# Kernel tuning notes

Hardware: AMD Instinct MI355X
Metric: run time of the kernel (lower is better)

## Reference

```python
import jax, jax.numpy as jnp
import numpy as np

QLEN, MLEN, BSZ, D_MODEL, N_HEAD, D_HEAD = 1024, 1024, 4, 1024, 16, 64
KLEN = QLEN + MLEN
LN_EPS = 1e-5


def _linear(x, W, b):
    return x @ W + b


def _layer_norm(x, g, b):
    mu = jnp.mean(x, axis=-1, keepdims=True)
    var = jnp.var(x, axis=-1, keepdims=True)
    return (x - mu) * jax.lax.rsqrt(var + LN_EPS) * g + b


def _rel_shift(x):
    # x: [b, n, q, k] -> Transformer-XL rel-shift via zero-pad + reshape trick
    b, n, q, k = x.shape
    x = jnp.pad(x, ((0, 0), (0, 0), (0, 0), (1, 0)))
    x = x.reshape(b, n, k + 1, q)[:, :, 1:, :].reshape(b, n, q, k)
    return x


def setup_inputs() -> dict:
    key = jax.random.key(0)
    ks = jax.random.split(key, 16)
    s = 0.02
    inp = {
        "w": jax.random.normal(ks[0], (QLEN, BSZ, D_MODEL), jnp.float32),
        "r": jax.random.normal(ks[1], (KLEN, D_MODEL), jnp.float32),
        "r_w_bias": jax.random.normal(ks[2], (N_HEAD, D_HEAD), jnp.float32) * s,
        "r_r_bias": jax.random.normal(ks[3], (N_HEAD, D_HEAD), jnp.float32) * s,
        "mems": jax.random.normal(ks[4], (MLEN, BSZ, D_MODEL), jnp.float32),
        "Wq": jax.random.normal(ks[5], (D_MODEL, N_HEAD * D_HEAD), jnp.float32) * s,
        "bq": jnp.zeros((N_HEAD * D_HEAD,), jnp.float32),
        "Wk": jax.random.normal(ks[6], (D_MODEL, N_HEAD * D_HEAD), jnp.float32) * s,
        "bk": jnp.zeros((N_HEAD * D_HEAD,), jnp.float32),
        "Wv": jax.random.normal(ks[7], (D_MODEL, N_HEAD * D_HEAD), jnp.float32) * s,
        "bv": jnp.zeros((N_HEAD * D_HEAD,), jnp.float32),
        "Wr": jax.random.normal(ks[8], (D_MODEL, N_HEAD * D_HEAD), jnp.float32) * s,
        "br": jnp.zeros((N_HEAD * D_HEAD,), jnp.float32),
        "Wo": jax.random.normal(ks[9], (N_HEAD * D_HEAD, D_MODEL), jnp.float32) * s,
        "bo": jnp.zeros((D_MODEL,), jnp.float32),
        "ln_g": jnp.ones((D_MODEL,), jnp.float32),
        "ln_b": jnp.zeros((D_MODEL,), jnp.float32),
    }
    # causal mask with memory: key j visible to query i iff j <= i + MLEN
    inp["attn_mask"] = jnp.arange(KLEN)[None, :] > (jnp.arange(QLEN)[:, None] + MLEN)
    return inp


def reference(w, r, r_w_bias, r_r_bias, mems, Wq, bq, Wk, bk, Wv, bv, Wr, br,
              Wo, bo, ln_g, ln_b, attn_mask):
    qlen, bsz = w.shape[0], w.shape[1]
    scale = 1.0 / (D_HEAD ** 0.5)

    cat = jnp.concatenate([mems, w], axis=0)               # [klen, b, d]
    klen = cat.shape[0]

    q = _linear(cat, Wq, bq)[-qlen:]                       # [q, b, n*d]
    k = _linear(cat, Wk, bk)                               # [k, b, n*d]
    v = _linear(cat, Wv, bv)
    rk = _linear(r, Wr, br)                                # [rlen, n*d]

    q = q.reshape(qlen, bsz, N_HEAD, D_HEAD)
    k = k.reshape(klen, bsz, N_HEAD, D_HEAD)
    v = v.reshape(klen, bsz, N_HEAD, D_HEAD)
    rk = rk.reshape(r.shape[0], N_HEAD, D_HEAD)

    AC = jnp.einsum('ibnd,jbnd->bnij', q + r_w_bias, k)
    BD = jnp.einsum('ibnd,jnd->bnij', q + r_r_bias, rk)
    BD = _rel_shift(BD)

    attn_score = scale * (AC + BD)                          # [b, n, q, k]
    attn_score = jnp.where(attn_mask[None, None, :, :], -jnp.inf, attn_score)
    attn_prob = jax.nn.softmax(attn_score, axis=3)

    attn_vec = jnp.einsum('bnij,jbnd->ibnd', attn_prob, v)
    attn_vec = attn_vec.reshape(qlen, bsz, N_HEAD * D_HEAD)
    attn_out = _linear(attn_vec, Wo, bo)

    return _layer_norm(w + attn_out, ln_g, ln_b)            # post-lnorm path
```

## Files before the change

kernel.cpp:

```cpp
#include <hip/hip_runtime.h>
#include <stdint.h>


typedef unsigned short u16;
typedef unsigned int u32;
typedef __attribute__((ext_vector_type(8))) short s16x8;
typedef __attribute__((ext_vector_type(4))) float f32x4;

typedef const __attribute__((address_space(1))) void gvoid;
typedef __attribute__((address_space(3))) void lvoid;

__device__ __forceinline__ void async16(const u16* g, u16* l) {
  __builtin_amdgcn_global_load_lds((gvoid*)g, (lvoid*)l, 16, 0, 0);
}

__device__ __forceinline__ float b2f(u16 h) {
  union { u32 u; float f; } v; v.u = ((u32)h) << 16; return v.f;
}
__device__ __forceinline__ u16 f2b(float f) {
  union { float f; u32 u; } v; v.f = f; u32 u = v.u;
  return (u16)((u + 0x7FFFu + ((u >> 16) & 1u)) >> 16);
}
__device__ __forceinline__ bool is_bf16(const u16* lng) { return lng[0] == 0x3F80u; }

__device__ __forceinline__ void ld8(const void* p, size_t idx, bool bf, u16* dst) {
  if (bf) {
    *(uint4*)dst = *(const uint4*)((const u16*)p + idx);
  } else {
    const float* f = (const float*)p + idx;
    float4 a = *(const float4*)f;
    float4 c = *(const float4*)(f + 4);
    dst[0] = f2b(a.x); dst[1] = f2b(a.y); dst[2] = f2b(a.z); dst[3] = f2b(a.w);
    dst[4] = f2b(c.x); dst[5] = f2b(c.y); dst[6] = f2b(c.z); dst[7] = f2b(c.w);
  }
}
__device__ __forceinline__ float ldS(const void* p, int idx, bool bf) {
  return bf ? b2f(((const u16*)p)[idx]) : ((const float*)p)[idx];
}

__device__ __forceinline__ void gemm_bt_body(
    u16* As, u16* Bs,
    const void* Alo, const void* Ahi, int splitRow,
    const u16* BT, const void* bias,
    const void* eb0, const void* eb1,
    u16* C0, u16* C1, bool bfin, bool abf,
    int bm, int bnc)
{
  const int t = threadIdx.x;
  const int lane = t & 63, w = t >> 6;
  const int wr = w >> 1, wc = w & 1;
  const int ml = lane & 15, q = lane >> 4;

  f32x4 zero4 = {0.f, 0.f, 0.f, 0.f};
  f32x4 acc[4][4];
#pragma unroll
  for (int i = 0; i < 4; ++i)
#pragma unroll
    for (int j = 0; j < 4; ++j) acc[i][j] = zero4;

  const int srow = t >> 3;
  const int scol = (((t & 7) ^ ((t >> 3) & 7)) << 3);
  const void* aptr[4]; size_t aidx[4]; const u16* bsrc[4];
#pragma unroll
  for (int p = 0; p < 4; ++p) {
    int gr = bm + p * 32 + srow;
    if (gr < splitRow) { aptr[p] = Alo; aidx[p] = (size_t)gr * 1024 + scol; }
    else { aptr[p] = Ahi; aidx[p] = (size_t)(gr - splitRow) * 1024 + scol; }
    bsrc[p] = BT + (size_t)(bnc + p * 32 + srow) * 1024 + scol;
  }

  for (int kk = 0; kk < 1024; kk += 64) {
    if (abf) {
      __syncthreads();
#pragma unroll
      for (int p = 0; p < 4; ++p) {
        async16((const u16*)aptr[p] + aidx[p] + kk, As + p * 2048 + t * 8);
        async16(bsrc[p] + kk, Bs + p * 2048 + t * 8);
      }
      __syncthreads();
    } else {
      u16 ta[4][8]; uint4 tb[4];
#pragma unroll
      for (int p = 0; p < 4; ++p) {
        ld8(aptr[p], aidx[p] + kk, false, ta[p]);
        tb[p] = *(const uint4*)(bsrc[p] + kk);
      }
      __syncthreads();
#pragma unroll
      for (int p = 0; p < 4; ++p) {
        *(uint4*)(As + p * 2048 + t * 8) = *(uint4*)ta[p];
        *(uint4*)(Bs + p * 2048 + t * 8) = tb[p];
      }
      __syncthreads();
    }
#pragma unroll
    for (int ki = 0; ki < 2; ++ki) {
      s16x8 af[4], bf[4];
#pragma unroll
      for (int mi = 0; mi < 4; ++mi) {
        int row = wr * 64 + mi * 16 + ml;
        af[mi] = *(const s16x8*)&As[row * 64 + ((((ki << 2) + q) ^ (ml & 7)) << 3)];
      }
#pragma unroll
      for (int ni = 0; ni < 4; ++ni) {
        int row = wc * 64 + ni * 16 + ml;
        bf[ni] = *(const s16x8*)&Bs[row * 64 + ((((ki << 2) + q) ^ (ml & 7)) << 3)];
      }
#pragma unroll
      for (int mi = 0; mi < 4; ++mi)
#pragma unroll
        for (int ni = 0; ni < 4; ++ni)
          acc[mi][ni] = __builtin_amdgcn_mfma_f32_16x16x32_bf16(af[mi], bf[ni],
                                                                acc[mi][ni], 0, 0, 0);
    }
  }

#pragma unroll
  for (int ni = 0; ni < 4; ++ni) {
    int gcol = bnc + wc * 64 + ni * 16 + ml;
    float bi = ldS(bias, gcol, bfin);
    float e0 = eb0 ? ldS(eb0, gcol, bfin) : 0.f;
    float e1 = eb1 ? ldS(eb1, gcol, bfin) : 0.f;
#pragma unroll
    for (int mi = 0; mi < 4; ++mi)
#pragma unroll
      for (int rr = 0; rr < 4; ++rr) {
        int grow = bm + wr * 64 + mi * 16 + 4 * q + rr;
        size_t off = (size_t)grow * 1024 + gcol;
        float v0 = acc[mi][ni][rr] + bi;
        if (C1) { C0[off] = f2b(v0 + e0); C1[off] = f2b(v0 + e1); }
        else    { C0[off] = f2b(v0); }
      }
  }
}

__device__ __forceinline__ void gemm_vt_body(
    u16* As, u16* Bs,
    const void* Mlo, const void* Whi,
    const u16* WvT, const void* bv,
    u16* vT, bool bfin,
    int j0, int nc0, int b)
{
  const int t = threadIdx.x;
  const int lane = t & 63, w = t >> 6;
  const int wr = w >> 1, wc = w & 1;
  const int ml = lane & 15, q = lane >> 4;

  f32x4 zero4 = {0.f, 0.f, 0.f, 0.f};
  f32x4 acc[4][4];
#pragma unroll
  for (int i = 0; i < 4; ++i)
#pragma unroll
    for (int j = 0; j < 4; ++j) acc[i][j] = zero4;

  const int srow = t >> 3;
  const int scol = (((t & 7) ^ ((t >> 3) & 7)) << 3);
  const u16* asrc[4]; const void* bptr[4]; size_t bidx[4];
#pragma unroll
  for (int p = 0; p < 4; ++p) {
    asrc[p] = WvT + (size_t)(nc0 + p * 32 + srow) * 1024 + scol;
    int j = j0 + p * 32 + srow;
    if (j < 1024) { bptr[p] = Mlo; bidx[p] = ((size_t)j * 4 + b) * 1024 + scol; }
    else { bptr[p] = Whi; bidx[p] = ((size_t)(j - 1024) * 4 + b) * 1024 + scol; }
  }

  for (int kk = 0; kk < 1024; kk += 64) {
    if (bfin) {
      __syncthreads();
#pragma unroll
      for (int p = 0; p < 4; ++p) {
        async16(asrc[p] + kk, As + p * 2048 + t * 8);
        async16((const u16*)bptr[p] + bidx[p] + kk, Bs + p * 2048 + t * 8);
      }
      __syncthreads();
    } else {
      u16 tb[4][8];
#pragma unroll
      for (int p = 0; p < 4; ++p) ld8(bptr[p], bidx[p] + kk, false, tb[p]);
      __syncthreads();
#pragma unroll
      for (int p = 0; p < 4; ++p) {
        async16(asrc[p] + kk, As + p * 2048 + t * 8);
        *(uint4*)(Bs + p * 2048 + t * 8) = *(uint4*)tb[p];
      }
      __syncthreads();
    }
#pragma unroll
    for (int ki = 0; ki < 2; ++ki) {
      s16x8 af[4], bf[4];
#pragma unroll
      for (int mi = 0; mi < 4; ++mi) {
        int row = wr * 64 + mi * 16 + ml;
        af[mi] = *(const s16x8*)&As[row * 64 + ((((ki << 2) + q) ^ (ml & 7)) << 3)];
      }
#pragma unroll
      for (int ni = 0; ni < 4; ++ni) {
        int row = wc * 64 + ni * 16 + ml;
        bf[ni] = *(const s16x8*)&Bs[row * 64 + ((((ki << 2) + q) ^ (ml & 7)) << 3)];
      }
#pragma unroll
      for (int mi = 0; mi < 4; ++mi)
#pragma unroll
        for (int ni = 0; ni < 4; ++ni)
          acc[mi][ni] = __builtin_amdgcn_mfma_f32_16x16x32_bf16(af[mi], bf[ni],
                                                                acc[mi][ni], 0, 0, 0);
    }
  }

#pragma unroll
  for (int mi = 0; mi < 4; ++mi)
#pragma unroll
    for (int rr = 0; rr < 4; ++rr) {
      int nc = nc0 + wr * 64 + mi * 16 + 4 * q + rr;
      float bi = ldS(bv, nc, bfin);
      size_t rbase = ((size_t)b * 1024 + nc) * 2048 + j0 + wc * 64 + ml * 4;
      u32 w0 = (u32)f2b(acc[mi][0][rr] + bi) | ((u32)f2b(acc[mi][1][rr] + bi) << 16);
      u32 w1 = (u32)f2b(acc[mi][2][rr] + bi) | ((u32)f2b(acc[mi][3][rr] + bi) << 16);
      uint2 pk; pk.x = w0; pk.y = w1;
      *(uint2*)(vT + rbase) = pk;
    }
}

__global__ __launch_bounds__(256) void gemm_bt(
    const void* __restrict__ Alo, const void* __restrict__ Ahi, int splitRow,
    const u16* __restrict__ BT, const void* __restrict__ bias,
    const void* __restrict__ eb0, const void* __restrict__ eb1,
    u16* __restrict__ C0, u16* __restrict__ C1,
    const u16* __restrict__ lng, int aIsInput)
{
  __shared__ u16 As[128 * 64];
  __shared__ u16 Bs[128 * 64];
  const bool bfin = is_bf16(lng);
  const bool abf = aIsInput ? bfin : true;
  gemm_bt_body(As, Bs, Alo, Ahi, splitRow, BT, bias, eb0, eb1, C0, C1,
               bfin, abf, blockIdx.y * 128, blockIdx.x * 128);
}

__global__ __launch_bounds__(256) void proj_uber(
    const void* __restrict__ mems, const void* __restrict__ w,
    const void* __restrict__ r,
    const u16* __restrict__ WkT, const void* __restrict__ bk,
    const u16* __restrict__ WvT, const void* __restrict__ bv,
    const u16* __restrict__ WqT, const void* __restrict__ bq,
    const void* __restrict__ rwb, const void* __restrict__ rrb,
    const u16* __restrict__ WrT, const void* __restrict__ br,
    u16* __restrict__ kb, u16* __restrict__ vT,
    u16* __restrict__ qw, u16* __restrict__ qr, u16* __restrict__ rkb,
    const u16* __restrict__ lng)
{
  __shared__ u16 As[128 * 64];
  __shared__ u16 Bs[128 * 64];
  const bool bfin = is_bf16(lng);
  int id = blockIdx.x;
  id = (id & 7) * 176 + (id >> 3);

  if (id < 512) {
    int bx = id & 7, by = id >> 3;
    gemm_bt_body(As, Bs, mems, w, 4096, WkT, bk, nullptr, nullptr,
                 kb, nullptr, bfin, bfin, by * 128, bx * 128);
  } else if (id < 1024) {
    int local = id - 512;
    int jx = local & 15, ny = (local >> 4) & 7, b = local >> 7;
    gemm_vt_body(As, Bs, mems, w, WvT, bv, vT, bfin, jx * 128, ny * 128, b);
  } else if (id < 1280) {
    int local = id - 1024;
    int bx = local & 7, by = local >> 3;
    gemm_bt_body(As, Bs, w, w, 4096, WqT, bq, rwb, rrb,
                 qw, qr, bfin, bfin, by * 128, bx * 128);
  } else {
    int local = id - 1280;
    int bx = local & 7, by = local >> 3;
    gemm_bt_body(As, Bs, r, r, 1 << 30, WrT, br, nullptr, nullptr,
                 rkb, nullptr, bfin, bfin, by * 128, bx * 128);
  }
}

__global__ __launch_bounds__(256) void transpose_w5(
    const void* __restrict__ W0, const void* __restrict__ W1,
    const void* __restrict__ W2, const void* __restrict__ W3,
    const void* __restrict__ W4,
    u16* __restrict__ T0, u16* __restrict__ T1, u16* __restrict__ T2,
    u16* __restrict__ T3, u16* __restrict__ T4, const u16* __restrict__ lng)
{
  __shared__ u16 tile[64 * 72];
  const bool bf = is_bf16(lng);
  const void* W; u16* T;
  switch (blockIdx.z) {
    case 0: W = W0; T = T0; break;
    case 1: W = W1; T = T1; break;
    case 2: W = W2; T = T2; break;
    case 3: W = W3; T = T3; break;
    default: W = W4; T = T4; break;
  }
  const int t = threadIdx.x;
  const int k0 = blockIdx.y * 64, n0 = blockIdx.x * 64;
#pragma unroll
  for (int p = 0; p < 2; ++p) {
    int s = p * 256 + t, row = s >> 3, ch = s & 7;
    u16 tmp[8];
    ld8(W, (size_t)(k0 + row) * 1024 + n0 + ch * 8, bf, tmp);
    *(uint4*)&tile[row * 72 + ch * 8] = *(uint4*)tmp;
  }
  __syncthreads();
#pragma unroll
  for (int p = 0; p < 2; ++p) {
    int s = p * 256 + t, nrow = s >> 3, ch = s & 7;
    union { u16 u[8]; uint4 v; } pk;
#pragma unroll
    for (int jj = 0; jj < 8; ++jj) pk.u[jj] = tile[(ch * 8 + jj) * 72 + nrow];
    *(uint4*)(T + (size_t)(n0 + nrow) * 1024 + k0 + ch * 8) = pk.v;
  }
}

__global__ __launch_bounds__(512, 4) void flash_attn(
    const u16* __restrict__ qw, const u16* __restrict__ qr,
    const u16* __restrict__ kb, const u16* __restrict__ vt,
    const u16* __restrict__ rkb, u16* __restrict__ av)
{
  constexpr int LP = 72;
  __shared__ u16 Ks[64 * LP];
  __shared__ u16 Vs[64 * LP];
  __shared__ u16 Rs[192 * LP];
  __shared__ u16 Ps[8][16 * LP];

  const int t = threadIdx.x;
  const int lane = t & 63, w = t >> 6;
  const int ml = lane & 15, q = lane >> 4;
  const int hbid = blockIdx.y * 8 + blockIdx.x;
  const int lbid = (hbid & 7) * 64 + (hbid >> 3);
  const int L = lbid & 63;
  const int i0idx = (L < 32) ? (L & 7) : 7 - (L & 7);
  const int i0 = i0idx * 128;
  const int bn = lbid >> 3, b = bn >> 4, nh = bn & 15;

  s16x8 aqw[2], aqr[2];
  {
    size_t qo = ((size_t)(i0 + 16 * w + ml) * 4 + b) * 1024 + nh * 64 + q * 8;
    aqw[0] = *(const s16x8*)(qw + qo);
    aqw[1] = *(const s16x8*)(qw + qo + 32);
    aqr[0] = *(const s16x8*)(qr + qo);
    aqr[1] = *(const s16x8*)(qr + qo + 32);
  }

  f32x4 zero4 = {0.f, 0.f, 0.f, 0.f};
  f32x4 o[4];
#pragma unroll
  for (int dt = 0; dt < 4; ++dt) o[dt] = zero4;
  float lsum[4] = {0.f, 0.f, 0.f, 0.f};

  const int ntiles = min(i0 / 64 + 18, 32);
  const int c_lo = 16 * (7 - w);
  const int srow = t >> 3, sch = t & 7;

  uint4 pK, pV, pR;
  auto issue_kv = [&](int jt) {
    const int j0n = jt * 64;
    pK = *(const uint4*)(kb + ((size_t)(j0n + srow) * 4 + b) * 1024 + nh * 64 + sch * 8);
    pV = *(const uint4*)(vt + ((size_t)bn * 64 + srow) * 2048 + j0n + sch * 8);
  };
  auto rload = [&](int g) {
    g = g < 0 ? 0 : (g > 2047 ? 2047 : g);
    return *(const uint4*)(rkb + (size_t)g * 1024 + nh * 64 + sch * 8);
  };

  {
    issue_kv(0);
    uint4 r0 = rload(896 - i0 + srow);
    uint4 r1 = rload(896 - i0 + srow + 64);
    uint4 r2 = rload(896 - i0 + srow + 128);
    *(uint4*)&Ks[srow * LP + sch * 8] = pK;
    *(uint4*)&Vs[srow * LP + sch * 8] = pV;
    *(uint4*)&Rs[(srow      ) * LP + sch * 8] = r0;
    *(uint4*)&Rs[(srow +  64) * LP + sch * 8] = r1;
    *(uint4*)&Rs[(srow + 128) * LP + sch * 8] = r2;
  }
  __syncthreads();

  int slab = 0;
  int rbase = c_lo;
  for (int jt = 0; jt < ntiles; ++jt) {
    const int j0 = jt * 64;
    if (jt > 0) {
      __syncthreads();
      *(uint4*)&Ks[srow * LP + sch * 8] = pK;
      *(uint4*)&Vs[srow * LP + sch * 8] = pV;
      *(uint4*)&Rs[(slab * 64 + srow) * LP + sch * 8] = pR;
      slab = slab == 2 ? 0 : slab + 1;
      rbase += 64; if (rbase >= 192) rbase -= 192;
      __syncthreads();
    }
    if (jt + 1 < ntiles) {
      issue_kv(jt + 1);
      pR = rload(64 * jt + 1088 - i0 + srow);
    }

    f32x4 sac[4];
#pragma unroll
    for (int tt = 0; tt < 4; ++tt) sac[tt] = zero4;
#pragma unroll
    for (int ki = 0; ki < 2; ++ki)
#pragma unroll
      for (int tt = 0; tt < 4; ++tt) {
        s16x8 bfr = *(const s16x8*)&Ks[(tt * 16 + ml) * LP + ki * 32 + q * 8];
        sac[tt] = __builtin_amdgcn_mfma_f32_16x16x32_bf16(aqw[ki], bfr, sac[tt], 0, 0, 0);
      }

    f32x4 g[5];
#pragma unroll
    for (int ct = 0; ct < 5; ++ct) g[ct] = zero4;
#pragma unroll
    for (int ct = 0; ct < 5; ++ct) {
      int pb = rbase + ct * 16; if (pb >= 192) pb -= 192;
      const u16* rp = &Rs[(pb + ml) * LP + q * 8];
      s16x8 b0 = *(const s16x8*)(rp);
      s16x8 b1 = *(const s16x8*)(rp + 32);
      g[ct] = __builtin_amdgcn_mfma_f32_16x16x32_bf16(aqr[0], b0, g[ct], 0, 0, 0);
      g[ct] = __builtin_amdgcn_mfma_f32_16x16x32_bf16(aqr[1], b1, g[ct], 0, 0, 0);
    }

    const bool mtile = (j0 + 63) > (i0 + 1024);

#pragma unroll
    for (int rr = 0; rr < 4; ++rr) {
      const int r = 4 * q + rr;
      const int irow = i0 + 16 * w + r;
      const int L2 = ((ml - r + 15) & 15) | (q << 4);
      const bool hs = ml < 15 - r;
      float bl0 = hs ? g[1][rr] : g[0][rr];
      float bl1 = hs ? g[2][rr] : g[1][rr];
      float bl2 = hs ? g[3][rr] : g[2][rr];
      float bl3 = hs ? g[4][rr] : g[3][rr];
      float band0 = __shfl(bl0, L2, 64);
      float band1 = __shfl(bl1, L2, 64);
      float band2 = __shfl(bl2, L2, 64);
      float band3 = __shfl(bl3, L2, 64);
      float s0 = 0.125f * (sac[0][rr] + band0);
      float s1 = 0.125f * (sac[1][rr] + band1);
      float s2 = 0.125f * (sac[2][rr] + band2);
      float s3 = 0.125f * (sac[3][rr] + band3);
      if (mtile) {
        int lim = irow + 1024 - j0 - ml;
        if (0 > lim)  s0 = -3.0e38f;
        if (16 > lim) s1 = -3.0e38f;
        if (32 > lim) s2 = -3.0e38f;
        if (48 > lim) s3 = -3.0e38f;
      }
      float p0 = __expf(s0), p1 = __expf(s1), p2 = __expf(s2), p3 = __expf(s3);
      lsum[rr] += (p0 + p1) + (p2 + p3);
      u32 w0 = (u32)f2b(p0) | ((u32)f2b(p1) << 16);
      u32 w1 = (u32)f2b(p2) | ((u32)f2b(p3) << 16);
      uint2 pk; pk.x = w0; pk.y = w1;
      *(uint2*)&Ps[w][r * LP + ml * 4] = pk;
    }

#pragma unroll
    for (int ki = 0; ki < 2; ++ki) {
      s16x8 a = *(const s16x8*)&Ps[w][ml * LP + ki * 32 + q * 8];
#pragma unroll
      for (int dt = 0; dt < 4; ++dt) {
        s16x8 bfr = *(const s16x8*)&Vs[(dt * 16 + ml) * LP + ki * 32 + q * 8];
        o[dt] = __builtin_amdgcn_mfma_f32_16x16x32_bf16(a, bfr, o[dt], 0, 0, 0);
      }
    }
  }

#pragma unroll
  for (int rr = 0; rr < 4; ++rr) {
    float l = lsum[rr];
#pragma unroll
    for (int off = 1; off < 16; off <<= 1) l += __shfl_xor(l, off);
    float inv = 1.f / l;
    int i = i0 + 16 * w + 4 * q + rr;
#pragma unroll
    for (int dt = 0; dt < 4; ++dt)
      av[((size_t)i * 4 + b) * 1024 + nh * 64 + dt * 16 + ml] = f2b(o[dt][rr] * inv);
  }
}

__global__ __launch_bounds__(256) void ln_kernel(
    const void* __restrict__ wi, const u16* __restrict__ ao,
    const void* __restrict__ gg, const void* __restrict__ bb,
    void* __restrict__ out)
{
  __shared__ float red[8];
  const bool bf = is_bf16((const u16*)gg);
  const int t = threadIdx.x;
  const int row = blockIdx.x;
  const int base = row * 1024 + t * 4;
  float x0, x1, x2, x3;
  if (bf) {
    ushort4 xw = *(const ushort4*)((const u16*)wi + base);
    x0 = b2f(xw.x); x1 = b2f(xw.y); x2 = b2f(xw.z); x3 = b2f(xw.w);
  } else {
    float4 xw = *(const float4*)((const float*)wi + base);
    x0 = xw.x; x1 = xw.y; x2 = xw.z; x3 = xw.w;
  }
  ushort4 xa = *(const ushort4*)(ao + base);
  x0 += b2f(xa.x); x1 += b2f(xa.y); x2 += b2f(xa.z); x3 += b2f(xa.w);
  float s = x0 + x1 + x2 + x3;
  float s2 = x0 * x0 + x1 * x1 + x2 * x2 + x3 * x3;
#pragma unroll
  for (int off = 1; off < 64; off <<= 1) {
    s += __shfl_xor(s, off);
    s2 += __shfl_xor(s2, off);
  }
  if ((t & 63) == 0) { red[t >> 6] = s; red[4 + (t >> 6)] = s2; }
  __syncthreads();
  float S = red[0] + red[1] + red[2] + red[3];
  float S2 = red[4] + red[5] + red[6] + red[7];
  float mu = S * (1.f / 1024.f);
  float var = S2 * (1.f / 1024.f) - mu * mu;
  float inv = rsqrtf(var + 1e-5f);
  float g0 = ldS(gg, t * 4 + 0, bf), g1 = ldS(gg, t * 4 + 1, bf);
  float g2 = ldS(gg, t * 4 + 2, bf), g3 = ldS(gg, t * 4 + 3, bf);
  float b0 = ldS(bb, t * 4 + 0, bf), b1 = ldS(bb, t * 4 + 1, bf);
  float b2v = ldS(bb, t * 4 + 2, bf), b3 = ldS(bb, t * 4 + 3, bf);
  float y0 = (x0 - mu) * inv * g0 + b0;
  float y1 = (x1 - mu) * inv * g1 + b1;
  float y2 = (x2 - mu) * inv * g2 + b2v;
  float y3 = (x3 - mu) * inv * g3 + b3;
  if (bf) {
    ushort4 r;
    r.x = f2b(y0); r.y = f2b(y1); r.z = f2b(y2); r.w = f2b(y3);
    *(ushort4*)((u16*)out + base) = r;
  } else {
    float4 r; r.x = y0; r.y = y1; r.z = y2; r.w = y3;
    *(float4*)((float*)out + base) = r;
  }
}

__global__ __launch_bounds__(256) void copy_w(
    const void* __restrict__ wi, const u16* __restrict__ lng,
    void* __restrict__ out)
{
  const bool bf = is_bf16(lng);
  int i = blockIdx.x * 256 + threadIdx.x;
  if (bf) ((u16*)out)[i] = ((const u16*)wi)[i];
  else    ((float*)out)[i] = ((const float*)wi)[i];
}

extern "C" void kernel_launch(void* const* d_in, const int* in_sizes, int n_in,
                              void* d_out, int out_size, void* d_ws, size_t ws_size,
                              hipStream_t stream) {
  (void)in_sizes; (void)n_in; (void)out_size;
  const void* w    = d_in[0];
  const void* r    = d_in[1];
  const void* rwb  = d_in[2];
  const void* rrb  = d_in[3];
  const void* mems = d_in[4];
  const void* Wq   = d_in[5];
  const void* bq   = d_in[6];
  const void* Wk   = d_in[7];
  const void* bk   = d_in[8];
  const void* Wv   = d_in[9];
  const void* bv   = d_in[10];
  const void* Wr   = d_in[11];
  const void* br   = d_in[12];
  const void* Wo   = d_in[13];
  const void* bo   = d_in[14];
  const u16*  lng  = (const u16*)d_in[15];
  const void* lnb  = d_in[16];

  dim3 blk(256);
  const size_t M = (size_t)1 << 20;
  const size_t NEED = 31 * M * 2;
  if (ws_size < NEED) {
    copy_w<<<dim3(16384), blk, 0, stream>>>(w, lng, d_out);
    return;
  }

  u16* ws  = (u16*)d_ws;
  u16* WqT = ws + 0 * M;
  u16* WkT = ws + 1 * M;
  u16* WvT = ws + 2 * M;
  u16* WrT = ws + 3 * M;
  u16* WoT = ws + 4 * M;
  u16* kb  = ws + 5 * M;
  u16* vT  = ws + 13 * M;
  u16* qw  = ws + 21 * M;
  u16* qr  = ws + 25 * M;
  u16* rkb = ws + 29 * M;
  u16* av  = ws + 0 * M;
  u16* ao  = qw;

  transpose_w5<<<dim3(16, 16, 5), blk, 0, stream>>>(Wq, Wk, Wv, Wr, Wo,
                                                    WqT, WkT, WvT, WrT, WoT, lng);
  proj_uber<<<dim3(1408), blk, 0, stream>>>(mems, w, r,
                                            WkT, bk, WvT, bv, WqT, bq, rwb, rrb,
                                            WrT, br, kb, vT, qw, qr, rkb, lng);
  flash_attn<<<dim3(8, 64), dim3(512), 0, stream>>>(qw, qr, kb, vT, rkb, av);
  gemm_bt<<<dim3(8, 32), blk, 0, stream>>>(av, av, 1 << 30, WoT, bo,
                                           nullptr, nullptr, ao, nullptr, lng, 0);
  ln_kernel<<<dim3(4096), blk, 0, stream>>>(w, ao, lng, lnb, d_out);
}
```

Baseline: 403.9 us.

## Use 256x256 tiles for projection GEMMs, retile output GEMM, add MFMA priority hints

```diff
diff --git a/kernel.cpp b/kernel.cpp
--- a/kernel.cpp
+++ b/kernel.cpp
@@ -38,7 +38,7 @@
   return bf ? b2f(((const u16*)p)[idx]) : ((const float*)p)[idx];
 }
 
-__device__ __forceinline__ void gemm_bt_body(
+__device__ __forceinline__ void gemm256_bt_body(
     u16* As, u16* Bs,
     const void* Alo, const void* Ahi, int splitRow,
     const u16* BT, const void* bias,
@@ -48,36 +48,38 @@
 {
   const int t = threadIdx.x;
   const int lane = t & 63, w = t >> 6;
-  const int wr = w >> 1, wc = w & 1;
+  const int wm = w >> 2, wn = w & 3;
   const int ml = lane & 15, q = lane >> 4;
 
   f32x4 zero4 = {0.f, 0.f, 0.f, 0.f};
-  f32x4 acc[4][4];
-#pragma unroll
-  for (int i = 0; i < 4; ++i)
+  f32x4 acc[8][4];
+#pragma unroll
+  for (int i = 0; i < 8; ++i)
 #pragma unroll
     for (int j = 0; j < 4; ++j) acc[i][j] = zero4;
 
   const int srow = t >> 3;
-  const int scol = (((t & 7) ^ ((t >> 3) & 7)) << 3);
+  const int scol = ((t & 7) ^ ((t >> 3) & 7)) << 3;
   const void* aptr[4]; size_t aidx[4]; const u16* bsrc[4];
 #pragma unroll
   for (int p = 0; p < 4; ++p) {
-    int gr = bm + p * 32 + srow;
+    int gr = bm + p * 64 + srow;
     if (gr < splitRow) { aptr[p] = Alo; aidx[p] = (size_t)gr * 1024 + scol; }
     else { aptr[p] = Ahi; aidx[p] = (size_t)(gr - splitRow) * 1024 + scol; }
-    bsrc[p] = BT + (size_t)(bnc + p * 32 + srow) * 1024 + scol;
-  }
+    bsrc[p] = BT + (size_t)(bnc + p * 64 + srow) * 1024 + scol;
+  }
+  u16* lA[4]; u16* lB[4];
+#pragma unroll
+  for (int p = 0; p < 4; ++p) { lA[p] = As + p * 4096 + t * 8; lB[p] = Bs + p * 4096 + t * 8; }
 
   for (int kk = 0; kk < 1024; kk += 64) {
+    __syncthreads();
     if (abf) {
-      __syncthreads();
 #pragma unroll
       for (int p = 0; p < 4; ++p) {
-        async16((const u16*)aptr[p] + aidx[p] + kk, As + p * 2048 + t * 8);
-        async16(bsrc[p] + kk, Bs + p * 2048 + t * 8);
-      }
-      __syncthreads();
+        async16((const u16*)aptr[p] + aidx[p] + kk, lA[p]);
+        async16(bsrc[p] + kk, lB[p]);
+      }
     } else {
       u16 ta[4][8]; uint4 tb[4];
 #pragma unroll
@@ -85,29 +87,25 @@
         ld8(aptr[p], aidx[p] + kk, false, ta[p]);
         tb[p] = *(const uint4*)(bsrc[p] + kk);
       }
-      __syncthreads();
 #pragma unroll
       for (int p = 0; p < 4; ++p) {
-        *(uint4*)(As + p * 2048 + t * 8) = *(uint4*)ta[p];
-        *(uint4*)(Bs + p * 2048 + t * 8) = tb[p];
-      }
-      __syncthreads();
-    }
+        *(uint4*)lA[p] = *(uint4*)ta[p];
+        *(uint4*)lB[p] = tb[p];
+      }
+    }
+    __syncthreads();
 #pragma unroll
     for (int ki = 0; ki < 2; ++ki) {
-      s16x8 af[4], bf[4];
-#pragma unroll
-      for (int mi = 0; mi < 4; ++mi) {
-        int row = wr * 64 + mi * 16 + ml;
-        af[mi] = *(const s16x8*)&As[row * 64 + ((((ki << 2) + q) ^ (ml & 7)) << 3)];
-      }
-#pragma unroll
-      for (int ni = 0; ni < 4; ++ni) {
-        int row = wc * 64 + ni * 16 + ml;
-        bf[ni] = *(const s16x8*)&Bs[row * 64 + ((((ki << 2) + q) ^ (ml & 7)) << 3)];
-      }
-#pragma unroll
-      for (int mi = 0; mi < 4; ++mi)
+      const int rc = (((ki << 2) + q) ^ (ml & 7)) << 3;
+      s16x8 af[8], bf[4];
+#pragma unroll
+      for (int mi = 0; mi < 8; ++mi)
+        af[mi] = *(const s16x8*)&As[(wm * 128 + mi * 16 + ml) * 64 + rc];
+#pragma unroll
+      for (int ni = 0; ni < 4; ++ni)
+        bf[ni] = *(const s16x8*)&Bs[(wn * 64 + ni * 16 + ml) * 64 + rc];
+#pragma unroll
+      for (int mi = 0; mi < 8; ++mi)
 #pragma unroll
         for (int ni = 0; ni < 4; ++ni)
           acc[mi][ni] = __builtin_amdgcn_mfma_f32_16x16x32_bf16(af[mi], bf[ni],
@@ -117,15 +115,15 @@
 
 #pragma unroll
   for (int ni = 0; ni < 4; ++ni) {
-    int gcol = bnc + wc * 64 + ni * 16 + ml;
+    int gcol = bnc + wn * 64 + ni * 16 + ml;
     float bi = ldS(bias, gcol, bfin);
     float e0 = eb0 ? ldS(eb0, gcol, bfin) : 0.f;
     float e1 = eb1 ? ldS(eb1, gcol, bfin) : 0.f;
 #pragma unroll
-    for (int mi = 0; mi < 4; ++mi)
+    for (int mi = 0; mi < 8; ++mi)
 #pragma unroll
       for (int rr = 0; rr < 4; ++rr) {
-        int grow = bm + wr * 64 + mi * 16 + 4 * q + rr;
+        int grow = bm + wm * 128 + mi * 16 + 4 * q + rr;
         size_t off = (size_t)grow * 1024 + gcol;
         float v0 = acc[mi][ni][rr] + bi;
         if (C1) { C0[off] = f2b(v0 + e0); C1[off] = f2b(v0 + e1); }
@@ -134,7 +132,7 @@
   }
 }
 
-__device__ __forceinline__ void gemm_vt_body(
+__device__ __forceinline__ void gemm256_vt_body(
     u16* As, u16* Bs,
     const void* Mlo, const void* Whi,
     const u16* WvT, const void* bv,
@@ -143,63 +141,61 @@
 {
   const int t = threadIdx.x;
   const int lane = t & 63, w = t >> 6;
-  const int wr = w >> 1, wc = w & 1;
+  const int wm = w >> 2, wn = w & 3;
   const int ml = lane & 15, q = lane >> 4;
 
   f32x4 zero4 = {0.f, 0.f, 0.f, 0.f};
-  f32x4 acc[4][4];
-#pragma unroll
-  for (int i = 0; i < 4; ++i)
+  f32x4 acc[8][4];
+#pragma unroll
+  for (int i = 0; i < 8; ++i)
 #pragma unroll
     for (int j = 0; j < 4; ++j) acc[i][j] = zero4;
 
   const int srow = t >> 3;
-  const int scol = (((t & 7) ^ ((t >> 3) & 7)) << 3);
+  const int scol = ((t & 7) ^ ((t >> 3) & 7)) << 3;
   const u16* asrc[4]; const void* bptr[4]; size_t bidx[4];
 #pragma unroll
   for (int p = 0; p < 4; ++p) {
-    asrc[p] = WvT + (size_t)(nc0 + p * 32 + srow) * 1024 + scol;
-    int j = j0 + p * 32 + srow;
+    asrc[p] = WvT + (size_t)(nc0 + p * 64 + srow) * 1024 + scol;
+    int j = j0 + p * 64 + srow;
     if (j < 1024) { bptr[p] = Mlo; bidx[p] = ((size_t)j * 4 + b) * 1024 + scol; }
     else { bptr[p] = Whi; bidx[p] = ((size_t)(j - 1024) * 4 + b) * 1024 + scol; }
   }
+  u16* lA[4]; u16* lB[4];
+#pragma unroll
+  for (int p = 0; p < 4; ++p) { lA[p] = As + p * 4096 + t * 8; lB[p] = Bs + p * 4096 + t * 8; }
 
   for (int kk = 0; kk < 1024; kk += 64) {
+    __syncthreads();
     if (bfin) {
-      __syncthreads();
 #pragma unroll
       for (int p = 0; p < 4; ++p) {
-        async16(asrc[p] + kk, As + p * 2048 + t * 8);
-        async16((const u16*)bptr[p] + bidx[p] + kk, Bs + p * 2048 + t * 8);
-      }
-      __syncthreads();
+        async16(asrc[p] + kk, lA[p]);
+        async16((const u16*)bptr[p] + bidx[p] + kk, lB[p]);
+      }
     } else {
       u16 tb[4][8];
 #pragma unroll
       for (int p = 0; p < 4; ++p) ld8(bptr[p], bidx[p] + kk, false, tb[p]);
-      __syncthreads();
 #pragma unroll
       for (int p = 0; p < 4; ++p) {
-        async16(asrc[p] + kk, As + p * 2048 + t * 8);
-        *(uint4*)(Bs + p * 2048 + t * 8) = *(uint4*)tb[p];
-      }
-      __syncthreads();
-    }
+        async16(asrc[p] + kk, lA[p]);
+        *(uint4*)lB[p] = *(uint4*)tb[p];
+      }
+    }
+    __syncthreads();
 #pragma unroll
     for (int ki = 0; ki < 2; ++ki) {
-      s16x8 af[4], bf[4];
-#pragma unroll
-      for (int mi = 0; mi < 4; ++mi) {
-        int row = wr * 64 + mi * 16 + ml;
-        af[mi] = *(const s16x8*)&As[row * 64 + ((((ki << 2) + q) ^ (ml & 7)) << 3)];
-      }
-#pragma unroll
-      for (int ni = 0; ni < 4; ++ni) {
-        int row = wc * 64 + ni * 16 + ml;
-        bf[ni] = *(const s16x8*)&Bs[row * 64 + ((((ki << 2) + q) ^ (ml & 7)) << 3)];
-      }
-#pragma unroll
-      for (int mi = 0; mi < 4; ++mi)
+      const int rc = (((ki << 2) + q) ^ (ml & 7)) << 3;
+      s16x8 af[8], bf[4];
+#pragma unroll
+      for (int mi = 0; mi < 8; ++mi)
+        af[mi] = *(const s16x8*)&As[(wm * 128 + mi * 16 + ml) * 64 + rc];
+#pragma unroll
+      for (int ni = 0; ni < 4; ++ni)
+        bf[ni] = *(const s16x8*)&Bs[(wn * 64 + ni * 16 + ml) * 64 + rc];
+#pragma unroll
+      for (int mi = 0; mi < 8; ++mi)
 #pragma unroll
         for (int ni = 0; ni < 4; ++ni)
           acc[mi][ni] = __builtin_amdgcn_mfma_f32_16x16x32_bf16(af[mi], bf[ni],
@@ -208,12 +204,12 @@
   }
 
 #pragma unroll
-  for (int mi = 0; mi < 4; ++mi)
+  for (int mi = 0; mi < 8; ++mi)
 #pragma unroll
     for (int rr = 0; rr < 4; ++rr) {
-      int nc = nc0 + wr * 64 + mi * 16 + 4 * q + rr;
+      int nc = nc0 + wm * 128 + mi * 16 + 4 * q + rr;
       float bi = ldS(bv, nc, bfin);
-      size_t rbase = ((size_t)b * 1024 + nc) * 2048 + j0 + wc * 64 + ml * 4;
+      size_t rbase = ((size_t)b * 1024 + nc) * 2048 + j0 + wn * 64 + ml * 4;
       u32 w0 = (u32)f2b(acc[mi][0][rr] + bi) | ((u32)f2b(acc[mi][1][rr] + bi) << 16);
       u32 w1 = (u32)f2b(acc[mi][2][rr] + bi) | ((u32)f2b(acc[mi][3][rr] + bi) << 16);
       uint2 pk; pk.x = w0; pk.y = w1;
@@ -221,22 +217,7 @@
     }
 }
 
-__global__ __launch_bounds__(256) void gemm_bt(
-    const void* __restrict__ Alo, const void* __restrict__ Ahi, int splitRow,
-    const u16* __restrict__ BT, const void* __restrict__ bias,
-    const void* __restrict__ eb0, const void* __restrict__ eb1,
-    u16* __restrict__ C0, u16* __restrict__ C1,
-    const u16* __restrict__ lng, int aIsInput)
-{
-  __shared__ u16 As[128 * 64];
-  __shared__ u16 Bs[128 * 64];
-  const bool bfin = is_bf16(lng);
-  const bool abf = aIsInput ? bfin : true;
-  gemm_bt_body(As, Bs, Alo, Ahi, splitRow, BT, bias, eb0, eb1, C0, C1,
-               bfin, abf, blockIdx.y * 128, blockIdx.x * 128);
-}
-
-__global__ __launch_bounds__(256) void proj_uber(
+__global__ __launch_bounds__(512, 2) void proj_uber256(
     const void* __restrict__ mems, const void* __restrict__ w,
     const void* __restrict__ r,
     const u16* __restrict__ WkT, const void* __restrict__ bk,
@@ -248,31 +229,139 @@
     u16* __restrict__ qw, u16* __restrict__ qr, u16* __restrict__ rkb,
     const u16* __restrict__ lng)
 {
-  __shared__ u16 As[128 * 64];
-  __shared__ u16 Bs[128 * 64];
+  __shared__ u16 As[256 * 64];
+  __shared__ u16 Bs[256 * 64];
   const bool bfin = is_bf16(lng);
   int id = blockIdx.x;
-  id = (id & 7) * 176 + (id >> 3);
-
-  if (id < 512) {
-    int bx = id & 7, by = id >> 3;
-    gemm_bt_body(As, Bs, mems, w, 4096, WkT, bk, nullptr, nullptr,
-                 kb, nullptr, bfin, bfin, by * 128, bx * 128);
-  } else if (id < 1024) {
-    int local = id - 512;
-    int jx = local & 15, ny = (local >> 4) & 7, b = local >> 7;
-    gemm_vt_body(As, Bs, mems, w, WvT, bv, vT, bfin, jx * 128, ny * 128, b);
-  } else if (id < 1280) {
-    int local = id - 1024;
-    int bx = local & 7, by = local >> 3;
-    gemm_bt_body(As, Bs, w, w, 4096, WqT, bq, rwb, rrb,
-                 qw, qr, bfin, bfin, by * 128, bx * 128);
+  id = (id & 7) * 44 + (id >> 3);
+
+  if (id < 128) {
+    int bx = id & 3, by = id >> 2;
+    gemm256_bt_body(As, Bs, mems, w, 4096, WkT, bk, nullptr, nullptr,
+                    kb, nullptr, bfin, bfin, by * 256, bx * 256);
+  } else if (id < 256) {
+    int local = id - 128;
+    int jx = local & 7, ny = (local >> 3) & 3, b = local >> 5;
+    gemm256_vt_body(As, Bs, mems, w, WvT, bv, vT, bfin, jx * 256, ny * 256, b);
+  } else if (id < 320) {
+    int local = id - 256;
+    int bx = local & 3, by = local >> 2;
+    gemm256_bt_body(As, Bs, w, w, 1 << 30, WqT, bq, rwb, rrb,
+                    qw, qr, bfin, bfin, by * 256, bx * 256);
   } else {
-    int local = id - 1280;
-    int bx = local & 7, by = local >> 3;
-    gemm_bt_body(As, Bs, r, r, 1 << 30, WrT, br, nullptr, nullptr,
-                 rkb, nullptr, bfin, bfin, by * 128, bx * 128);
-  }
+    int local = id - 320;
+    int bx = local & 3, by = local >> 2;
+    gemm256_bt_body(As, Bs, r, r, 1 << 30, WrT, br, nullptr, nullptr,
+                    rkb, nullptr, bfin, bfin, by * 256, bx * 256);
+  }
+}
+
+__device__ __forceinline__ void gemm_bt_body(
+    u16* As, u16* Bs,
+    const void* Alo, const void* Ahi, int splitRow,
+    const u16* BT, const void* bias,
+    const void* eb0, const void* eb1,
+    u16* C0, u16* C1, bool bfin, bool abf,
+    int bm, int bnc)
+{
+  const int t = threadIdx.x;
+  const int lane = t & 63, w = t >> 6;
+  const int wr = w >> 1, wc = w & 1;
+  const int ml = lane & 15, q = lane >> 4;
+
+  f32x4 zero4 = {0.f, 0.f, 0.f, 0.f};
+  f32x4 acc[4][4];
+#pragma unroll
+  for (int i = 0; i < 4; ++i)
+#pragma unroll
+    for (int j = 0; j < 4; ++j) acc[i][j] = zero4;
+
+  const int srow = t >> 2;
+  const int sch  = t & 3;
+  const void* aptr[2]; size_t aidx[2]; const u16* bsrc[2];
+#pragma unroll
+  for (int p = 0; p < 2; ++p) {
+    int gr = bm + srow + p * 64;
+    if (gr < splitRow) { aptr[p] = Alo; aidx[p] = (size_t)gr * 1024 + sch * 8; }
+    else { aptr[p] = Ahi; aidx[p] = (size_t)(gr - splitRow) * 1024 + sch * 8; }
+    bsrc[p] = BT + (size_t)(bnc + srow + p * 64) * 1024 + sch * 8;
+  }
+  u16* lA[2] = { As + t * 8, As + 2048 + t * 8 };
+  u16* lB[2] = { Bs + t * 8, Bs + 2048 + t * 8 };
+
+  for (int kk = 0; kk < 1024; kk += 32) {
+    if (abf) {
+      __syncthreads();
+      async16((const u16*)aptr[0] + aidx[0] + kk, lA[0]);
+      async16((const u16*)aptr[1] + aidx[1] + kk, lA[1]);
+      async16(bsrc[0] + kk, lB[0]);
+      async16(bsrc[1] + kk, lB[1]);
+      __syncthreads();
+    } else {
+      u16 ta0[8], ta1[8];
+      ld8(aptr[0], aidx[0] + kk, false, ta0);
+      ld8(aptr[1], aidx[1] + kk, false, ta1);
+      uint4 vb0 = *(const uint4*)(bsrc[0] + kk);
+      uint4 vb1 = *(const uint4*)(bsrc[1] + kk);
+      __syncthreads();
+      *(uint4*)lA[0] = *(uint4*)ta0;
+      *(uint4*)lA[1] = *(uint4*)ta1;
+      *(uint4*)lB[0] = vb0;
+      *(uint4*)lB[1] = vb1;
+      __syncthreads();
+    }
+    s16x8 af[4], bf[4];
+#pragma unroll
+    for (int mi = 0; mi < 4; ++mi)
+      af[mi] = *(const s16x8*)&As[(wr * 64 + mi * 16 + ml) * 32 + q * 8];
+#pragma unroll
+    for (int ni = 0; ni < 4; ++ni)
+      bf[ni] = *(const s16x8*)&Bs[(wc * 64 + ni * 16 + ml) * 32 + q * 8];
+#pragma unroll
+    for (int mi = 0; mi < 4; ++mi)
+#pragma unroll
+      for (int ni = 0; ni < 4; ++ni)
+        acc[mi][ni] = __builtin_amdgcn_mfma_f32_16x16x32_bf16(af[mi], bf[ni],
+                                                              acc[mi][ni], 0, 0, 0);
+  }
+
+#pragma unroll
+  for (int ni = 0; ni < 4; ++ni) {
+    int gcol = bnc + wc * 64 + ni * 16 + ml;
+    float bi = ldS(bias, gcol, bfin);
+    float e0 = eb0 ? ldS(eb0, gcol, bfin) : 0.f;
+    float e1 = eb1 ? ldS(eb1, gcol, bfin) : 0.f;
+#pragma unroll
+    for (int mi = 0; mi < 4; ++mi)
+#pragma unroll
+      for (int rr = 0; rr < 4; ++rr) {
+        int grow = bm + wr * 64 + mi * 16 + 4 * q + rr;
+        size_t off = (size_t)grow * 1024 + gcol;
+        float v0 = acc[mi][ni][rr] + bi;
+        if (C1) { C0[off] = f2b(v0 + e0); C1[off] = f2b(v0 + e1); }
+        else    { C0[off] = f2b(v0); }
+      }
+  }
+}
+
+__global__ __launch_bounds__(256) void gemm_bt(
+    const void* __restrict__ Alo, const void* __restrict__ Ahi, int splitRow,
+    const u16* __restrict__ BT, const void* __restrict__ bias,
+    const void* __restrict__ eb0, const void* __restrict__ eb1,
+    u16* __restrict__ C0, u16* __restrict__ C1,
+    const u16* __restrict__ lng, int aIsInput)
+{
+  __shared__ u16 As[128 * 32];
+  __shared__ u16 Bs[128 * 32];
+  const bool bfin = is_bf16(lng);
+  const bool abf = aIsInput ? bfin : true;
+  int lin = blockIdx.y * gridDim.x + blockIdx.x;
+  int nwg = gridDim.x * gridDim.y;
+  int cpx = nwg >> 3;
+  int id  = (lin & 7) * cpx + (lin >> 3);
+  int bx = id % gridDim.x, by = id / gridDim.x;
+  gemm_bt_body(As, Bs, Alo, Ahi, splitRow, BT, bias, eb0, eb1, C0, C1,
+               bfin, abf, by * 128, bx * 128);
 }
 
 __global__ __launch_bounds__(256) void transpose_w5(
@@ -394,6 +483,7 @@
       pR = rload(64 * jt + 1088 - i0 + srow);
     }
 
+    __builtin_amdgcn_s_setprio(1);
     f32x4 sac[4];
 #pragma unroll
     for (int tt = 0; tt < 4; ++tt) sac[tt] = zero4;
@@ -417,6 +507,7 @@
       g[ct] = __builtin_amdgcn_mfma_f32_16x16x32_bf16(aqr[0], b0, g[ct], 0, 0, 0);
       g[ct] = __builtin_amdgcn_mfma_f32_16x16x32_bf16(aqr[1], b1, g[ct], 0, 0, 0);
     }
+    __builtin_amdgcn_s_setprio(0);
 
     const bool mtile = (j0 + 63) > (i0 + 1024);
 
@@ -453,6 +544,7 @@
       *(uint2*)&Ps[w][r * LP + ml * 4] = pk;
     }
 
+    __builtin_amdgcn_s_setprio(1);
 #pragma unroll
     for (int ki = 0; ki < 2; ++ki) {
       s16x8 a = *(const s16x8*)&Ps[w][ml * LP + ki * 32 + q * 8];
@@ -462,6 +554,7 @@
         o[dt] = __builtin_amdgcn_mfma_f32_16x16x32_bf16(a, bfr, o[dt], 0, 0, 0);
       }
     }
+    __builtin_amdgcn_s_setprio(0);
   }
 
 #pragma unroll
@@ -585,9 +678,10 @@
 
   transpose_w5<<<dim3(16, 16, 5), blk, 0, stream>>>(Wq, Wk, Wv, Wr, Wo,
                                                     WqT, WkT, WvT, WrT, WoT, lng);
-  proj_uber<<<dim3(1408), blk, 0, stream>>>(mems, w, r,
-                                            WkT, bk, WvT, bv, WqT, bq, rwb, rrb,
-                                            WrT, br, kb, vT, qw, qr, rkb, lng);
+  proj_uber256<<<dim3(352), dim3(512), 0, stream>>>(mems, w, r,
+                                                    WkT, bk, WvT, bv, WqT, bq,
+                                                    rwb, rrb, WrT, br,
+                                                    kb, vT, qw, qr, rkb, lng);
   flash_attn<<<dim3(8, 64), dim3(512), 0, stream>>>(qw, qr, kb, vT, rkb, av);
   gemm_bt<<<dim3(8, 32), blk, 0, stream>>>(av, av, 1 << 30, WoT, bo,
                                            nullptr, nullptr, ao, nullptr, lng, 0);
```

Measured after the change: 357.4 us. 1.13x faster.
